# Performance work log

Hardware: AMD Instinct MI355X
Metric: run time of the kernel (lower is better)

## Reference

```python
import jax, jax.numpy as jnp
import numpy as np

FEAT_DIM = 256
HEAD_DIM = 32
N_HEADS = FEAT_DIM // HEAD_DIM
SIZE = 8  # sqrt(max_seq_len)
P = SIZE * SIZE  # 64
B, G = 4, 1024


def _rel_pos_index(size: int) -> np.ndarray:
    coords = np.stack(np.meshgrid(np.arange(size), np.arange(size), indexing='ij'))
    flat = coords.reshape(2, -1)
    rel = flat[:, :, None] - flat[:, None, :]
    rel = rel.transpose(1, 2, 0).copy()
    rel[:, :, 0] += size - 1
    rel[:, :, 1] += size - 1
    rel[:, :, 0] *= 2 * size - 1
    return rel.sum(-1)  # [P, P], values in [0, (2*size-1)^2)


def setup_inputs() -> dict:
    key = jax.random.key(0)
    ks = jax.random.split(key, 6)
    d = FEAT_DIM
    w_std = d ** -0.5
    return {
        'x': jax.random.normal(ks[0], (B, G, P, d), dtype=jnp.float32),
        'Wqkv': jax.random.normal(ks[1], (d, 3 * d), dtype=jnp.float32) * w_std,
        'bqkv': jnp.zeros((3 * d,), dtype=jnp.float32),
        'Wm': jax.random.normal(ks[2], (d, d), dtype=jnp.float32) * w_std,
        'bm': jnp.zeros((d,), dtype=jnp.float32),
        'bias_table': jax.random.normal(ks[3], ((2 * SIZE - 1) ** 2, N_HEADS), dtype=jnp.float32) * 0.02,
        'rel_index': jnp.asarray(_rel_pos_index(SIZE), dtype=jnp.int32),
    }


def reference(x, Wqkv, bqkv, Wm, bm, bias_table, rel_index):
    Bb, Gg, Pp, D = x.shape
    H, DH = N_HEADS, HEAD_DIM
    scale = D ** -0.5  # note: scale uses feat_dim, as in the original
    qkv = x @ Wqkv + bqkv  # [B,G,P,3D]
    q, k, v = jnp.split(qkv, 3, axis=-1)
    q = q.reshape(Bb, Gg, Pp, H, DH)
    k = k.reshape(Bb, Gg, Pp, H, DH) * scale
    v = v.reshape(Bb, Gg, Pp, H, DH)
    scores = jnp.einsum('BGIHD,BGJHD->BGHIJ', q, k)  # [B,G,H,P,P]
    # gathered relative-position bias: [P,P,H] -> [1,1,H,P,P]
    bias = bias_table[rel_index]  # [P,P,H]
    bias = jnp.transpose(bias, (2, 0, 1))[None, None]  # [1,1,H,P,P]
    attn = jax.nn.softmax(scores + bias, axis=-1)
    out = jnp.einsum('BGHIJ,BGJHD->BGIHD', attn, v)
    out = out.reshape(Bb, Gg, Pp, D)
    return out @ Wm + bm
```

## Files before the change

kernel.cpp:

```cpp
#include <hip/hip_runtime.h>

typedef short short8 __attribute__((ext_vector_type(8)));
typedef float f32x4 __attribute__((ext_vector_type(4)));

#define D_FEAT 256
#define P_TOK  64

#define XB_OFF 0
#define SCR_OFF 16896
#define LDS_TOT 37376
#define STX 264
#define ST40 40
#define ST72 72

static __device__ __forceinline__ unsigned short f2b(float f) {
  union { float f; unsigned u; } v; v.f = f;
  unsigned r = v.u + 0x7FFFu + ((v.u >> 16) & 1u);
  return (unsigned short)(r >> 16);
}

__global__ void prep_w_kernel(const float* __restrict__ W, unsigned short* __restrict__ Wf,
                              int ncols, int total, int qkv) {
  const int tid = blockIdx.x * blockDim.x + threadIdx.x;
  if (tid >= total) return;
  const int l  = tid & 63;
  const int ks = (tid >> 6) & 7;
  const int nt = tid >> 9;
  int col;
  if (qkv) {
    const int wv = nt / 6, tt = nt % 6;
    col = (tt >> 1) * 256 + wv * 32 + (tt & 1) * 16 + (l & 15);
  } else {
    col = nt * 16 + (l & 15);
  }
  const int k0 = ks * 32 + (l >> 4) * 8;
  short8 v;
#pragma unroll
  for (int j = 0; j < 8; ++j) v[j] = (short)f2b(W[(size_t)(k0 + j) * ncols + col]);
  *reinterpret_cast<short8*>(&Wf[(size_t)tid * 8]) = v;
}

__global__ void prep_bias_kernel(const float* __restrict__ bt, const int* __restrict__ ri,
                                 float* __restrict__ bc) {
  const int tid = blockIdx.x * blockDim.x + threadIdx.x;
  if (tid >= 8192) return;
  const int l  = tid & 63;
  const int t  = (tid >> 6) & 15;
  const int h  = tid >> 10;
  const int mt = t >> 2, nt = t & 3;
  f32x4 v;
#pragma unroll
  for (int i = 0; i < 4; ++i) {
    const int r = mt * 16 + (l >> 4) * 4 + i;
    const int c = nt * 16 + (l & 15);
    v[i] = bt[ri[r * 64 + c] * 8 + h];
  }
  *reinterpret_cast<f32x4*>(&bc[(size_t)tid * 4]) = v;
}

__global__ __launch_bounds__(512, 4)
void win_attn_kernel(const float* __restrict__ x,
                     const float* __restrict__ bqkv,
                     const float* __restrict__ bm,
                     const unsigned short* __restrict__ Wqkv_f,
                     const unsigned short* __restrict__ Wm_f,
                     const float* __restrict__ bias_c,
                     float* __restrict__ out)
{
  __shared__ unsigned short sm[LDS_TOT];
  const int tid = threadIdx.x;
  const int w   = tid >> 6;
  const int l   = tid & 63;
  const int lr  = l & 15;
  const int lg  = l >> 4;
  const long long win = blockIdx.x;
  const float* xw = x + win * (P_TOK * D_FEAT);
  const int SW = SCR_OFF + w * 2560;

#pragma unroll
  for (int it = 0; it < 8; ++it) {
    const int f = it * 2048 + tid * 4;
    const int row = f >> 8, col = f & 255;
    const float4 v = *reinterpret_cast<const float4*>(xw + f);
    ushort4 b;
    b.x = f2b(v.x); b.y = f2b(v.y); b.z = f2b(v.z); b.w = f2b(v.w);
    *reinterpret_cast<ushort4*>(&sm[XB_OFF + row * STX + col]) = b;
  }
  __syncthreads();

  short8 qf[4], kf[4], vf[2][2];
#pragma unroll
  for (int m = 0; m < 3; ++m) {
    f32x4 acc[4][2];
    {
      float bb0 = bqkv[m * 256 + w * 32 + lr];
      float bb1 = bqkv[m * 256 + w * 32 + 16 + lr];
#pragma unroll
      for (int mt = 0; mt < 4; ++mt) {
        acc[mt][0] = (f32x4){bb0, bb0, bb0, bb0};
        acc[mt][1] = (f32x4){bb1, bb1, bb1, bb1};
      }
    }
#pragma unroll
    for (int ks = 0; ks < 8; ++ks) {
      short8 a[4];
#pragma unroll
      for (int mt = 0; mt < 4; ++mt)
        a[mt] = *reinterpret_cast<const short8*>(
            &sm[XB_OFF + (lr + 16 * mt) * STX + lg * 8 + ks * 32]);
#pragma unroll
      for (int sub = 0; sub < 2; ++sub) {
        const short8 bf = *reinterpret_cast<const short8*>(
            &Wqkv_f[(size_t)(((w * 6 + m * 2 + sub) * 8 + ks) * 64 + l) * 8]);
#pragma unroll
        for (int mt = 0; mt < 4; ++mt)
          acc[mt][sub] = __builtin_amdgcn_mfma_f32_16x16x32_bf16(a[mt], bf, acc[mt][sub], 0, 0, 0);
      }
    }

    if (m == 2) {
#pragma unroll
      for (int sub = 0; sub < 2; ++sub)
#pragma unroll
        for (int mt = 0; mt < 4; ++mt) {
          ushort4 b;
          b.x = f2b(acc[mt][sub][0]); b.y = f2b(acc[mt][sub][1]);
          b.z = f2b(acc[mt][sub][2]); b.w = f2b(acc[mt][sub][3]);
          *reinterpret_cast<ushort4*>(&sm[SW + (sub * 16 + lr) * ST72 + 16 * mt + 4 * lg]) = b;
        }
#pragma unroll
      for (int nt = 0; nt < 2; ++nt)
#pragma unroll
        for (int kh = 0; kh < 2; ++kh)
          vf[nt][kh] = *reinterpret_cast<const short8*>(
              &sm[SW + (lr + 16 * nt) * ST72 + kh * 32 + lg * 8]);
    } else {
      const float sc = (m == 1) ? 0.0625f : 1.0f;
#pragma unroll
      for (int sub = 0; sub < 2; ++sub)
#pragma unroll
        for (int mt = 0; mt < 4; ++mt)
#pragma unroll
          for (int i = 0; i < 4; ++i)
            sm[SW + (16 * mt + 4 * lg + i) * ST40 + sub * 16 + lr] = f2b(acc[mt][sub][i] * sc);
#pragma unroll
      for (int mt = 0; mt < 4; ++mt) {
        const short8 fr = *reinterpret_cast<const short8*>(
            &sm[SW + (lr + 16 * mt) * ST40 + lg * 8]);
        if (m == 0) qf[mt] = fr; else kf[mt] = fr;
      }
    }
  }

  f32x4 s[4][4];
#pragma unroll
  for (int mt = 0; mt < 4; ++mt)
#pragma unroll
    for (int nt = 0; nt < 4; ++nt) {
      const f32x4 bb = *reinterpret_cast<const f32x4*>(
          &bias_c[(size_t)((w * 16 + mt * 4 + nt) * 64 + l) * 4]);
      s[mt][nt] = __builtin_amdgcn_mfma_f32_16x16x32_bf16(qf[mt], kf[nt], bb, 0, 0, 0);
    }
#pragma unroll
  for (int mt = 0; mt < 4; ++mt)
#pragma unroll
    for (int i = 0; i < 4; ++i) {
      float mx = fmaxf(fmaxf(s[mt][0][i], s[mt][1][i]), fmaxf(s[mt][2][i], s[mt][3][i]));
      mx = fmaxf(mx, __shfl_xor(mx, 1));
      mx = fmaxf(mx, __shfl_xor(mx, 2));
      mx = fmaxf(mx, __shfl_xor(mx, 4));
      mx = fmaxf(mx, __shfl_xor(mx, 8));
      float e0 = __expf(s[mt][0][i] - mx);
      float e1 = __expf(s[mt][1][i] - mx);
      float e2 = __expf(s[mt][2][i] - mx);
      float e3 = __expf(s[mt][3][i] - mx);
      float sum = e0 + e1 + e2 + e3;
      sum += __shfl_xor(sum, 1);
      sum += __shfl_xor(sum, 2);
      sum += __shfl_xor(sum, 4);
      sum += __shfl_xor(sum, 8);
      const float rinv = 1.0f / sum;
      s[mt][0][i] = e0 * rinv; s[mt][1][i] = e1 * rinv;
      s[mt][2][i] = e2 * rinv; s[mt][3][i] = e3 * rinv;
    }

  f32x4 o[4][2];
#pragma unroll
  for (int mt = 0; mt < 4; ++mt)
#pragma unroll
    for (int nt = 0; nt < 2; ++nt)
      o[mt][nt] = (f32x4){0.f, 0.f, 0.f, 0.f};
#pragma unroll
  for (int kh = 0; kh < 2; ++kh) {
#pragma unroll
    for (int ntl = 0; ntl < 2; ++ntl)
#pragma unroll
      for (int mt = 0; mt < 4; ++mt)
#pragma unroll
        for (int i = 0; i < 4; ++i)
          sm[SW + (16 * mt + 4 * lg + i) * ST40 + ntl * 16 + lr] = f2b(s[mt][2 * kh + ntl][i]);
#pragma unroll
    for (int mt = 0; mt < 4; ++mt) {
      const short8 pa = *reinterpret_cast<const short8*>(
          &sm[SW + (lr + 16 * mt) * ST40 + lg * 8]);
#pragma unroll
      for (int nt = 0; nt < 2; ++nt)
        o[mt][nt] = __builtin_amdgcn_mfma_f32_16x16x32_bf16(pa, vf[nt][kh], o[mt][nt], 0, 0, 0);
    }
  }

  __syncthreads();
#pragma unroll
  for (int mt = 0; mt < 4; ++mt)
#pragma unroll
    for (int nt = 0; nt < 2; ++nt)
#pragma unroll
      for (int i = 0; i < 4; ++i)
        sm[XB_OFF + (16 * mt + 4 * lg + i) * STX + w * 32 + nt * 16 + lr] = f2b(o[mt][nt][i]);
  __syncthreads();

  f32x4 po[4][2];
  {
    float bm0 = bm[w * 32 + lr];
    float bm1 = bm[w * 32 + 16 + lr];
#pragma unroll
    for (int mt = 0; mt < 4; ++mt) {
      po[mt][0] = (f32x4){bm0, bm0, bm0, bm0};
      po[mt][1] = (f32x4){bm1, bm1, bm1, bm1};
    }
  }
#pragma unroll
  for (int ks = 0; ks < 8; ++ks) {
    short8 a[4];
#pragma unroll
    for (int mt = 0; mt < 4; ++mt)
      a[mt] = *reinterpret_cast<const short8*>(
          &sm[XB_OFF + (lr + 16 * mt) * STX + lg * 8 + ks * 32]);
#pragma unroll
    for (int nt = 0; nt < 2; ++nt) {
      const short8 bf = *reinterpret_cast<const short8*>(
          &Wm_f[(size_t)(((w * 2 + nt) * 8 + ks) * 64 + l) * 8]);
#pragma unroll
      for (int mt = 0; mt < 4; ++mt)
        po[mt][nt] = __builtin_amdgcn_mfma_f32_16x16x32_bf16(a[mt], bf, po[mt][nt], 0, 0, 0);
    }
  }

  float* ow = out + win * (P_TOK * D_FEAT);
#pragma unroll
  for (int mt = 0; mt < 4; ++mt)
#pragma unroll
    for (int nt = 0; nt < 2; ++nt)
#pragma unroll
      for (int i = 0; i < 4; ++i)
        ow[(16 * mt + 4 * lg + i) * 256 + w * 32 + nt * 16 + lr] = po[mt][nt][i];
}

extern "C" void kernel_launch(void* const* d_in, const int* in_sizes, int n_in,
                              void* d_out, int out_size, void* d_ws, size_t ws_size,
                              hipStream_t stream) {
  const float* x    = (const float*)d_in[0];
  const float* Wqkv = (const float*)d_in[1];
  const float* bqkv = (const float*)d_in[2];
  const float* Wm   = (const float*)d_in[3];
  const float* bm   = (const float*)d_in[4];
  const float* bt   = (const float*)d_in[5];
  const int*   ri   = (const int*)d_in[6];

  unsigned short* Wqkv_f = (unsigned short*)d_ws;
  unsigned short* Wm_f   = (unsigned short*)((char*)d_ws + 393216);
  float*          bias_c = (float*)((char*)d_ws + 524288);

  prep_w_kernel<<<48, 512, 0, stream>>>(Wqkv, Wqkv_f, 768, 24576, 1);
  prep_w_kernel<<<16, 512, 0, stream>>>(Wm, Wm_f, 256, 8192, 0);
  prep_bias_kernel<<<16, 512, 0, stream>>>(bt, ri, bias_c);

  const int nwin = in_sizes[0] / (P_TOK * D_FEAT);
  win_attn_kernel<<<nwin, 512, 0, stream>>>(x, bqkv, bm, Wqkv_f, Wm_f, bias_c, (float*)d_out);
}
```

Before: 262.1 us.

## Transpose MFMA operand roles for vectorized stores and column-wise softmax

Swaps the A/B operands in the Q/K projection, the score matmul and the output projection, so accumulators hold transposed tiles. This lets LDS and global writes use packed 8-byte and 16-byte vector stores instead of scalar ones, and softmax reduces over registers with fewer cross-lane shuffles. The K scale is folded into the weight prep, and the relative-bias gather is transposed to match. It also uses the packed bf16 conversion intrinsic. The risk is the extra register pressure from larger accumulator sets under the 512-thread, 4-block launch bound.

Result: slower. 308.0 us (+17.5%).

```diff
diff --git a/kernel.cpp b/kernel.cpp
--- a/kernel.cpp
+++ b/kernel.cpp
@@ -1,10 +1,8 @@
 #include <hip/hip_runtime.h>
+#include <hip/hip_bf16.h>
 
 typedef short short8 __attribute__((ext_vector_type(8)));
 typedef float f32x4 __attribute__((ext_vector_type(4)));
-
-#define D_FEAT 256
-#define P_TOK  64
 
 #define XB_OFF 0
 #define SCR_OFF 16896
@@ -17,6 +15,11 @@
   union { float f; unsigned u; } v; v.f = f;
   unsigned r = v.u + 0x7FFFu + ((v.u >> 16) & 1u);
   return (unsigned short)(r >> 16);
+}
+static __device__ __forceinline__ unsigned pk2(float a, float b) {
+  union { __hip_bfloat162 h; unsigned u; } v;
+  v.h = __float22bfloat162_rn(make_float2(a, b));
+  return v.u;
 }
 
 __global__ void prep_w_kernel(const float* __restrict__ W, unsigned short* __restrict__ Wf,
@@ -26,17 +29,18 @@
   const int l  = tid & 63;
   const int ks = (tid >> 6) & 7;
   const int nt = tid >> 9;
-  int col;
+  int col; float scl = 1.0f;
   if (qkv) {
     const int wv = nt / 6, tt = nt % 6;
     col = (tt >> 1) * 256 + wv * 32 + (tt & 1) * 16 + (l & 15);
+    if ((tt >> 1) == 1) scl = 0.0625f;
   } else {
     col = nt * 16 + (l & 15);
   }
   const int k0 = ks * 32 + (l >> 4) * 8;
   short8 v;
 #pragma unroll
-  for (int j = 0; j < 8; ++j) v[j] = (short)f2b(W[(size_t)(k0 + j) * ncols + col]);
+  for (int j = 0; j < 8; ++j) v[j] = (short)f2b(W[(size_t)(k0 + j) * ncols + col] * scl);
   *reinterpret_cast<short8*>(&Wf[(size_t)tid * 8]) = v;
 }
 
@@ -53,7 +57,7 @@
   for (int i = 0; i < 4; ++i) {
     const int r = mt * 16 + (l >> 4) * 4 + i;
     const int c = nt * 16 + (l & 15);
-    v[i] = bt[ri[r * 64 + c] * 8 + h];
+    v[i] = bt[ri[c * 64 + r] * 8 + h];
   }
   *reinterpret_cast<f32x4*>(&bc[(size_t)tid * 4]) = v;
 }
@@ -74,7 +78,7 @@
   const int lr  = l & 15;
   const int lg  = l >> 4;
   const long long win = blockIdx.x;
-  const float* xw = x + win * (P_TOK * D_FEAT);
+  const float* xw = x + win * 16384;
   const int SW = SCR_OFF + w * 2560;
 
 #pragma unroll
@@ -82,74 +86,99 @@
     const int f = it * 2048 + tid * 4;
     const int row = f >> 8, col = f & 255;
     const float4 v = *reinterpret_cast<const float4*>(xw + f);
-    ushort4 b;
-    b.x = f2b(v.x); b.y = f2b(v.y); b.z = f2b(v.z); b.w = f2b(v.w);
-    *reinterpret_cast<ushort4*>(&sm[XB_OFF + row * STX + col]) = b;
+    *reinterpret_cast<uint2*>(&sm[XB_OFF + row * STX + col]) =
+        make_uint2(pk2(v.x, v.y), pk2(v.z, v.w));
   }
   __syncthreads();
 
-  short8 qf[4], kf[4], vf[2][2];
-#pragma unroll
-  for (int m = 0; m < 3; ++m) {
-    f32x4 acc[4][2];
-    {
-      float bb0 = bqkv[m * 256 + w * 32 + lr];
-      float bb1 = bqkv[m * 256 + w * 32 + 16 + lr];
-#pragma unroll
-      for (int mt = 0; mt < 4; ++mt) {
-        acc[mt][0] = (f32x4){bb0, bb0, bb0, bb0};
-        acc[mt][1] = (f32x4){bb1, bb1, bb1, bb1};
+  short8 qf[4], kf[4];
+  {
+    f32x4 aqk[4][4];
+#pragma unroll
+    for (int ms = 0; ms < 4; ++ms) {
+      f32x4 bi = *reinterpret_cast<const f32x4*>(
+          &bqkv[(ms >> 1) * 256 + w * 32 + (ms & 1) * 16 + 4 * lg]);
+      if (ms >= 2) bi *= 0.0625f;
+#pragma unroll
+      for (int nt = 0; nt < 4; ++nt) aqk[ms][nt] = bi;
+    }
+#pragma unroll
+    for (int ks = 0; ks < 8; ++ks) {
+      short8 bx[4];
+#pragma unroll
+      for (int nt = 0; nt < 4; ++nt)
+        bx[nt] = *reinterpret_cast<const short8*>(
+            &sm[XB_OFF + (lr + 16 * nt) * STX + lg * 8 + ks * 32]);
+#pragma unroll
+      for (int ms = 0; ms < 4; ++ms) {
+        const short8 af = *reinterpret_cast<const short8*>(
+            &Wqkv_f[(size_t)(((w * 6 + ms) * 8 + ks) * 64 + l) * 8]);
+#pragma unroll
+        for (int nt = 0; nt < 4; ++nt)
+          aqk[ms][nt] = __builtin_amdgcn_mfma_f32_16x16x32_bf16(af, bx[nt], aqk[ms][nt], 0, 0, 0);
       }
     }
 #pragma unroll
+    for (int sub = 0; sub < 2; ++sub)
+#pragma unroll
+      for (int nt = 0; nt < 4; ++nt)
+        *reinterpret_cast<uint2*>(&sm[SW + (lr + 16 * nt) * ST40 + sub * 16 + 4 * lg]) =
+            make_uint2(pk2(aqk[sub][nt][0], aqk[sub][nt][1]),
+                       pk2(aqk[sub][nt][2], aqk[sub][nt][3]));
+#pragma unroll
+    for (int t = 0; t < 4; ++t)
+      qf[t] = *reinterpret_cast<const short8*>(&sm[SW + (lr + 16 * t) * ST40 + lg * 8]);
+#pragma unroll
+    for (int sub = 0; sub < 2; ++sub)
+#pragma unroll
+      for (int nt = 0; nt < 4; ++nt)
+        *reinterpret_cast<uint2*>(&sm[SW + (lr + 16 * nt) * ST40 + sub * 16 + 4 * lg]) =
+            make_uint2(pk2(aqk[2 + sub][nt][0], aqk[2 + sub][nt][1]),
+                       pk2(aqk[2 + sub][nt][2], aqk[2 + sub][nt][3]));
+#pragma unroll
+    for (int t = 0; t < 4; ++t)
+      kf[t] = *reinterpret_cast<const short8*>(&sm[SW + (lr + 16 * t) * ST40 + lg * 8]);
+  }
+
+  short8 vf[2][2];
+  {
+    f32x4 av[4][2];
+    const float b0 = bqkv[512 + w * 32 + lr];
+    const float b1 = bqkv[512 + w * 32 + 16 + lr];
+#pragma unroll
+    for (int mt = 0; mt < 4; ++mt) {
+      av[mt][0] = (f32x4){b0, b0, b0, b0};
+      av[mt][1] = (f32x4){b1, b1, b1, b1};
+    }
+#pragma unroll
     for (int ks = 0; ks < 8; ++ks) {
-      short8 a[4];
+      short8 ax[4];
 #pragma unroll
       for (int mt = 0; mt < 4; ++mt)
-        a[mt] = *reinterpret_cast<const short8*>(
+        ax[mt] = *reinterpret_cast<const short8*>(
             &sm[XB_OFF + (lr + 16 * mt) * STX + lg * 8 + ks * 32]);
 #pragma unroll
       for (int sub = 0; sub < 2; ++sub) {
-        const short8 bf = *reinterpret_cast<const short8*>(
-            &Wqkv_f[(size_t)(((w * 6 + m * 2 + sub) * 8 + ks) * 64 + l) * 8]);
+        const short8 bw = *reinterpret_cast<const short8*>(
+            &Wqkv_f[(size_t)(((w * 6 + 4 + sub) * 8 + ks) * 64 + l) * 8]);
 #pragma unroll
         for (int mt = 0; mt < 4; ++mt)
-          acc[mt][sub] = __builtin_amdgcn_mfma_f32_16x16x32_bf16(a[mt], bf, acc[mt][sub], 0, 0, 0);
+          av[mt][sub] = __builtin_amdgcn_mfma_f32_16x16x32_bf16(ax[mt], bw, av[mt][sub], 0, 0, 0);
       }
     }
-
-    if (m == 2) {
+#pragma unroll
+    for (int mt = 0; mt < 4; ++mt)
 #pragma unroll
       for (int sub = 0; sub < 2; ++sub)
-#pragma unroll
-        for (int mt = 0; mt < 4; ++mt) {
-          ushort4 b;
-          b.x = f2b(acc[mt][sub][0]); b.y = f2b(acc[mt][sub][1]);
-          b.z = f2b(acc[mt][sub][2]); b.w = f2b(acc[mt][sub][3]);
-          *reinterpret_cast<ushort4*>(&sm[SW + (sub * 16 + lr) * ST72 + 16 * mt + 4 * lg]) = b;
-        }
-#pragma unroll
-      for (int nt = 0; nt < 2; ++nt)
-#pragma unroll
-        for (int kh = 0; kh < 2; ++kh)
-          vf[nt][kh] = *reinterpret_cast<const short8*>(
-              &sm[SW + (lr + 16 * nt) * ST72 + kh * 32 + lg * 8]);
-    } else {
-      const float sc = (m == 1) ? 0.0625f : 1.0f;
-#pragma unroll
-      for (int sub = 0; sub < 2; ++sub)
-#pragma unroll
-        for (int mt = 0; mt < 4; ++mt)
-#pragma unroll
-          for (int i = 0; i < 4; ++i)
-            sm[SW + (16 * mt + 4 * lg + i) * ST40 + sub * 16 + lr] = f2b(acc[mt][sub][i] * sc);
-#pragma unroll
-      for (int mt = 0; mt < 4; ++mt) {
-        const short8 fr = *reinterpret_cast<const short8*>(
-            &sm[SW + (lr + 16 * mt) * ST40 + lg * 8]);
-        if (m == 0) qf[mt] = fr; else kf[mt] = fr;
-      }
-    }
+        *reinterpret_cast<uint2*>(&sm[SW + (sub * 16 + lr) * ST72 + 16 * mt + 4 * lg]) =
+            make_uint2(pk2(av[mt][sub][0], av[mt][sub][1]),
+                       pk2(av[mt][sub][2], av[mt][sub][3]));
+#pragma unroll
+    for (int nt = 0; nt < 2; ++nt)
+#pragma unroll
+      for (int kh = 0; kh < 2; ++kh)
+        vf[nt][kh] = *reinterpret_cast<const short8*>(
+            &sm[SW + (lr + 16 * nt) * ST72 + kh * 32 + lg * 8]);
   }
 
   f32x4 s[4][4];
@@ -159,46 +188,48 @@
     for (int nt = 0; nt < 4; ++nt) {
       const f32x4 bb = *reinterpret_cast<const f32x4*>(
           &bias_c[(size_t)((w * 16 + mt * 4 + nt) * 64 + l) * 4]);
-      s[mt][nt] = __builtin_amdgcn_mfma_f32_16x16x32_bf16(qf[mt], kf[nt], bb, 0, 0, 0);
-    }
+      s[mt][nt] = __builtin_amdgcn_mfma_f32_16x16x32_bf16(kf[mt], qf[nt], bb, 0, 0, 0);
+    }
+  float rs[4];
+#pragma unroll
+  for (int nt = 0; nt < 4; ++nt) {
+    float mx = s[0][nt][0];
+#pragma unroll
+    for (int mt = 0; mt < 4; ++mt)
+#pragma unroll
+      for (int i = 0; i < 4; ++i) mx = fmaxf(mx, s[mt][nt][i]);
+    mx = fmaxf(mx, __shfl_xor(mx, 16));
+    mx = fmaxf(mx, __shfl_xor(mx, 32));
+    float sum = 0.f;
+#pragma unroll
+    for (int mt = 0; mt < 4; ++mt)
+#pragma unroll
+      for (int i = 0; i < 4; ++i) {
+        const float e = __expf(s[mt][nt][i] - mx);
+        s[mt][nt][i] = e;
+        sum += e;
+      }
+    sum += __shfl_xor(sum, 16);
+    sum += __shfl_xor(sum, 32);
+    rs[nt] = 1.0f / sum;
+  }
+
+  f32x4 o[4][2];
 #pragma unroll
   for (int mt = 0; mt < 4; ++mt)
 #pragma unroll
-    for (int i = 0; i < 4; ++i) {
-      float mx = fmaxf(fmaxf(s[mt][0][i], s[mt][1][i]), fmaxf(s[mt][2][i], s[mt][3][i]));
-      mx = fmaxf(mx, __shfl_xor(mx, 1));
-      mx = fmaxf(mx, __shfl_xor(mx, 2));
-      mx = fmaxf(mx, __shfl_xor(mx, 4));
-      mx = fmaxf(mx, __shfl_xor(mx, 8));
-      float e0 = __expf(s[mt][0][i] - mx);
-      float e1 = __expf(s[mt][1][i] - mx);
-      float e2 = __expf(s[mt][2][i] - mx);
-      float e3 = __expf(s[mt][3][i] - mx);
-      float sum = e0 + e1 + e2 + e3;
-      sum += __shfl_xor(sum, 1);
-      sum += __shfl_xor(sum, 2);
-      sum += __shfl_xor(sum, 4);
-      sum += __shfl_xor(sum, 8);
-      const float rinv = 1.0f / sum;
-      s[mt][0][i] = e0 * rinv; s[mt][1][i] = e1 * rinv;
-      s[mt][2][i] = e2 * rinv; s[mt][3][i] = e3 * rinv;
-    }
-
-  f32x4 o[4][2];
-#pragma unroll
-  for (int mt = 0; mt < 4; ++mt)
-#pragma unroll
-    for (int nt = 0; nt < 2; ++nt)
-      o[mt][nt] = (f32x4){0.f, 0.f, 0.f, 0.f};
+    for (int nt = 0; nt < 2; ++nt) o[mt][nt] = (f32x4){0.f, 0.f, 0.f, 0.f};
 #pragma unroll
   for (int kh = 0; kh < 2; ++kh) {
 #pragma unroll
-    for (int ntl = 0; ntl < 2; ++ntl)
-#pragma unroll
-      for (int mt = 0; mt < 4; ++mt)
-#pragma unroll
-        for (int i = 0; i < 4; ++i)
-          sm[SW + (16 * mt + 4 * lg + i) * ST40 + ntl * 16 + lr] = f2b(s[mt][2 * kh + ntl][i]);
+    for (int mtl = 0; mtl < 2; ++mtl)
+#pragma unroll
+      for (int nt = 0; nt < 4; ++nt) {
+        const int mt = 2 * kh + mtl;
+        *reinterpret_cast<uint2*>(&sm[SW + (lr + 16 * nt) * ST40 + mtl * 16 + 4 * lg]) =
+            make_uint2(pk2(s[mt][nt][0] * rs[nt], s[mt][nt][1] * rs[nt]),
+                       pk2(s[mt][nt][2] * rs[nt], s[mt][nt][3] * rs[nt]));
+      }
 #pragma unroll
     for (int mt = 0; mt < 4; ++mt) {
       const short8 pa = *reinterpret_cast<const short8*>(
@@ -219,41 +250,35 @@
         sm[XB_OFF + (16 * mt + 4 * lg + i) * STX + w * 32 + nt * 16 + lr] = f2b(o[mt][nt][i]);
   __syncthreads();
 
-  f32x4 po[4][2];
-  {
-    float bm0 = bm[w * 32 + lr];
-    float bm1 = bm[w * 32 + 16 + lr];
-#pragma unroll
-    for (int mt = 0; mt < 4; ++mt) {
-      po[mt][0] = (f32x4){bm0, bm0, bm0, bm0};
-      po[mt][1] = (f32x4){bm1, bm1, bm1, bm1};
-    }
+  f32x4 po[2][4];
+#pragma unroll
+  for (int mt = 0; mt < 2; ++mt) {
+    const f32x4 bi = *reinterpret_cast<const f32x4*>(&bm[w * 32 + mt * 16 + 4 * lg]);
+#pragma unroll
+    for (int nt = 0; nt < 4; ++nt) po[mt][nt] = bi;
   }
 #pragma unroll
   for (int ks = 0; ks < 8; ++ks) {
-    short8 a[4];
-#pragma unroll
-    for (int mt = 0; mt < 4; ++mt)
-      a[mt] = *reinterpret_cast<const short8*>(
-          &sm[XB_OFF + (lr + 16 * mt) * STX + lg * 8 + ks * 32]);
-#pragma unroll
-    for (int nt = 0; nt < 2; ++nt) {
-      const short8 bf = *reinterpret_cast<const short8*>(
-          &Wm_f[(size_t)(((w * 2 + nt) * 8 + ks) * 64 + l) * 8]);
-#pragma unroll
-      for (int mt = 0; mt < 4; ++mt)
-        po[mt][nt] = __builtin_amdgcn_mfma_f32_16x16x32_bf16(a[mt], bf, po[mt][nt], 0, 0, 0);
-    }
-  }
-
-  float* ow = out + win * (P_TOK * D_FEAT);
-#pragma unroll
-  for (int mt = 0; mt < 4; ++mt)
-#pragma unroll
-    for (int nt = 0; nt < 2; ++nt)
-#pragma unroll
-      for (int i = 0; i < 4; ++i)
-        ow[(16 * mt + 4 * lg + i) * 256 + w * 32 + nt * 16 + lr] = po[mt][nt][i];
+    short8 bx[4];
+#pragma unroll
+    for (int nt = 0; nt < 4; ++nt)
+      bx[nt] = *reinterpret_cast<const short8*>(
+          &sm[XB_OFF + (lr + 16 * nt) * STX + lg * 8 + ks * 32]);
+#pragma unroll
+    for (int mt = 0; mt < 2; ++mt) {
+      const short8 af = *reinterpret_cast<const short8*>(
+          &Wm_f[(size_t)(((w * 2 + mt) * 8 + ks) * 64 + l) * 8]);
+#pragma unroll
+      for (int nt = 0; nt < 4; ++nt)
+        po[mt][nt] = __builtin_amdgcn_mfma_f32_16x16x32_bf16(af, bx[nt], po[mt][nt], 0, 0, 0);
+    }
+  }
+  float* ow = out + win * 16384;
+#pragma unroll
+  for (int mt = 0; mt < 2; ++mt)
+#pragma unroll
+    for (int nt = 0; nt < 4; ++nt)
+      *reinterpret_cast<f32x4*>(&ow[(lr + 16 * nt) * 256 + w * 32 + mt * 16 + 4 * lg]) = po[mt][nt];
 }
 
 extern "C" void kernel_launch(void* const* d_in, const int* in_sizes, int n_in,
@@ -275,6 +300,6 @@
   prep_w_kernel<<<16, 512, 0, stream>>>(Wm, Wm_f, 256, 8192, 0);
   prep_bias_kernel<<<16, 512, 0, stream>>>(bt, ri, bias_c);
 
-  const int nwin = in_sizes[0] / (P_TOK * D_FEAT);
+  const int nwin = in_sizes[0] / 16384;
   win_attn_kernel<<<nwin, 512, 0, stream>>>(x, bqkv, bm, Wqkv_f, Wm_f, bias_c, (float*)d_out);
 }
```
